# Kernel tuning notes

Hardware: AMD Instinct MI355X
Metric: run time of the kernel (lower is better)

Reference implementation:

```python
import jax, jax.numpy as jnp
import numpy as np

N_NODES = 50000
N_EDGES = 800000
NODE_DIM = 256
EDGE_DIM = 64
NUM_REL = 4
HID = 512      # hidden_dims[0]
LAST = 128     # last_dim_size
BATCH = 16384
EPS = 1e-10    # torchdrug RelationalGraphConv degree-normalization eps


def _glorot(k, shape):
    fan_in = shape[-1]
    return jax.random.normal(k, shape, jnp.float32) / np.sqrt(fan_in).astype(np.float32)


def setup_inputs() -> dict:
    key = jax.random.key(0)
    ks = jax.random.split(key, 20)
    inp = {}
    inp["inputs"] = jax.random.randint(ks[0], (BATCH, 3), 0, N_NODES, dtype=jnp.int32)
    inp["node_feature"] = jax.random.normal(ks[1], (N_NODES, NODE_DIM), jnp.float32)
    inp["edge_feature"] = jax.random.normal(ks[2], (N_EDGES, EDGE_DIM), jnp.float32)
    inp["edge_src"] = jax.random.randint(ks[3], (N_EDGES,), 0, N_NODES, dtype=jnp.int32)
    inp["edge_dst"] = jax.random.randint(ks[4], (N_EDGES,), 0, N_NODES, dtype=jnp.int32)
    inp["edge_rel"] = jax.random.randint(ks[5], (N_EDGES,), 0, NUM_REL, dtype=jnp.int32)
    # RGCN layer 1: 256 -> 512
    inp["We1"] = _glorot(ks[6], (NODE_DIM, EDGE_DIM)); inp["be1"] = jnp.zeros((NODE_DIM,), jnp.float32)
    inp["Wl1"] = _glorot(ks[7], (HID, NUM_REL * NODE_DIM)); inp["bl1"] = jnp.zeros((HID,), jnp.float32)
    inp["Ws1"] = _glorot(ks[8], (HID, NODE_DIM)); inp["bs1"] = jnp.zeros((HID,), jnp.float32)
    # RGCN layer 2: 512 -> 128
    inp["We2"] = _glorot(ks[9], (HID, EDGE_DIM)); inp["be2"] = jnp.zeros((HID,), jnp.float32)
    inp["Wl2"] = _glorot(ks[10], (LAST, NUM_REL * HID)); inp["bl2"] = jnp.zeros((LAST,), jnp.float32)
    inp["Ws2"] = _glorot(ks[11], (LAST, HID)); inp["bs2"] = jnp.zeros((LAST,), jnp.float32)
    # ccle_mlp: edge_dim -> 256 -> 128
    inp["Wc1"] = _glorot(ks[12], (256, EDGE_DIM)); inp["bc1"] = jnp.zeros((256,), jnp.float32)
    inp["Wc2"] = _glorot(ks[13], (LAST, 256)); inp["bc2"] = jnp.zeros((LAST,), jnp.float32)
    # final MLP: 3*128 -> 128 -> 64 -> 1
    inp["Wf1"] = _glorot(ks[14], (128, 3 * LAST)); inp["bf1"] = jnp.zeros((128,), jnp.float32)
    inp["Wf2"] = _glorot(ks[15], (64, 128)); inp["bf2"] = jnp.zeros((64,), jnp.float32)
    inp["Wf3"] = _glorot(ks[16], (1, 64)); inp["bf3"] = jnp.zeros((1,), jnp.float32)
    return inp


def _rgcn_layer(x, edge_src, edge_dst, edge_rel, edge_feat, We, be, Wl, bl, Ws, bs):
    """torchdrug RelationalGraphConv: message = x[src] + edge_linear(edge_feat);
    per-(node,relation) mean aggregation; combine = linear(update) + self_loop(x); relu."""
    in_dim = x.shape[1]
    msg = x[edge_src] + edge_feat @ We.T + be                      # [E, in_dim]
    seg = edge_dst * NUM_REL + edge_rel                            # [E]
    agg = jax.ops.segment_sum(msg, seg, num_segments=N_NODES * NUM_REL)
    cnt = jax.ops.segment_sum(jnp.ones((msg.shape[0], 1), msg.dtype), seg,
                              num_segments=N_NODES * NUM_REL)
    upd = (agg / (cnt + EPS)).reshape(N_NODES, NUM_REL * in_dim)   # [N, R*in_dim]
    return jax.nn.relu(upd @ Wl.T + bl + x @ Ws.T + bs)


def reference(inputs, node_feature, edge_feature, edge_src, edge_dst, edge_rel,
              We1, be1, Wl1, bl1, Ws1, bs1,
              We2, be2, Wl2, bl2, Ws2, bs2,
              Wc1, bc1, Wc2, bc2,
              Wf1, bf1, Wf2, bf2, Wf3, bf3):
    d1, d2, ctx = inputs[:, 0], inputs[:, 1], inputs[:, 2]
    h = _rgcn_layer(node_feature, edge_src, edge_dst, edge_rel, edge_feature,
                    We1, be1, Wl1, bl1, Ws1, bs1)
    h = _rgcn_layer(h, edge_src, edge_dst, edge_rel, edge_feature,
                    We2, be2, Wl2, bl2, Ws2, bs2)
    x1 = h[d1]                                                     # [B, 128]
    x2 = h[d2]                                                     # [B, 128]
    ef = edge_feature[ctx]                                         # [B, 64]
    x3 = jax.nn.relu(ef @ Wc1.T + bc1) @ Wc2.T + bc2               # [B, 128]
    x = jnp.concatenate([x1, x2, x3], axis=1)                      # [B, 384]
    x = jax.nn.relu(x @ Wf1.T + bf1)
    x = jax.nn.relu(x @ Wf2.T + bf2)
    return x @ Wf3.T + bf3                                         # [B, 1]
```

## Files before the change

kernel.cpp:

```cpp
#include <hip/hip_runtime.h>
#include <hip/hip_bf16.h>

#define N_NODES 50000
#define N_EDGES 800000
#define NODE_DIM 256
#define EDGE_DIM 64
#define NUM_REL 4
#define HID 512
#define LAST 128
#define BATCH 16384
#define EPS 1e-10f
#define NSEG (N_NODES * NUM_REL)

#define K1 1600
#define K2 832

typedef __bf16 bf16_t;
typedef __attribute__((ext_vector_type(8))) __bf16 bf16x8;
typedef __attribute__((ext_vector_type(4))) __bf16 bf16x4;
typedef __attribute__((ext_vector_type(2))) __bf16 bf16x2;
typedef __attribute__((ext_vector_type(4))) float f32x4;

typedef __attribute__((address_space(1))) const unsigned int g_u32;
typedef __attribute__((address_space(3))) unsigned int l_u32;
static __device__ __forceinline__ void gload16(const void* g, void* l) {
    __builtin_amdgcn_global_load_lds((g_u32*)g, (l_u32*)l, 16, 0, 0);
}

__global__ __launch_bounds__(256) void hist_kernel(
    const int* __restrict__ edst, const int* __restrict__ erel, int* __restrict__ hist)
{
    int e = blockIdx.x * 256 + threadIdx.x;
    if (e >= N_EDGES) return;
    atomicAdd(&hist[edst[e] * NUM_REL + erel[e]], 1);
}

#define SCAN_B 2048
__global__ __launch_bounds__(256) void scan1(
    const int* __restrict__ in, int* __restrict__ out, int* __restrict__ bsum, int n)
{
    __shared__ int sh[256];
    int base = blockIdx.x * SCAN_B + threadIdx.x * 8;
    int v[8]; int s = 0;
#pragma unroll
    for (int i = 0; i < 8; ++i) {
        int idx = base + i;
        v[i] = s;
        s += (idx < n) ? in[idx] : 0;
    }
    sh[threadIdx.x] = s;
    __syncthreads();
    for (int off = 1; off < 256; off <<= 1) {
        int t = (threadIdx.x >= off) ? sh[threadIdx.x - off] : 0;
        __syncthreads();
        sh[threadIdx.x] += t;
        __syncthreads();
    }
    int texcl = (threadIdx.x == 0) ? 0 : sh[threadIdx.x - 1];
#pragma unroll
    for (int i = 0; i < 8; ++i) {
        int idx = base + i;
        if (idx < n) out[idx] = texcl + v[i];
    }
    if (threadIdx.x == 255) bsum[blockIdx.x] = sh[255];
}

__global__ void scan2(int* bsum, int nb)
{
    if (threadIdx.x == 0 && blockIdx.x == 0) {
        int s = 0;
        for (int i = 0; i < nb; ++i) { int t = bsum[i]; bsum[i] = s; s += t; }
    }
}

__global__ __launch_bounds__(256) void scan3(int* __restrict__ out, const int* __restrict__ bsum, int n)
{
    int idx = blockIdx.x * SCAN_B + threadIdx.x * 8;
    int add = bsum[blockIdx.x];
#pragma unroll
    for (int i = 0; i < 8; ++i)
        if (idx + i < n) out[idx + i] += add;
}

__global__ __launch_bounds__(256) void csr_fill(
    const int* __restrict__ edst, const int* __restrict__ erel, const int* __restrict__ esrc,
    const int* __restrict__ offs, int* __restrict__ cursor,
    int* __restrict__ csr_src, int* __restrict__ csr_eid)
{
    int e = blockIdx.x * 256 + threadIdx.x;
    if (e >= N_EDGES) return;
    int seg = edst[e] * NUM_REL + erel[e];
    int pos = offs[seg] + atomicAdd(&cursor[seg], 1);
    csr_src[pos] = esrc[e];
    csr_eid[pos] = e;
}

__global__ __launch_bounds__(256) void prep_small(
    const float* __restrict__ Wc1, const float* __restrict__ Wc2,
    const float* __restrict__ Wf1, const float* __restrict__ Wf2,
    const float* __restrict__ bl1, const float* __restrict__ bs1,
    const float* __restrict__ bl2, const float* __restrict__ bs2,
    bf16_t* __restrict__ Wc1b, bf16_t* __restrict__ Wc2b,
    bf16_t* __restrict__ Wf1b, bf16_t* __restrict__ Wf2b,
    float* __restrict__ bias12, float* __restrict__ bias22)
{
    int i = blockIdx.x * 256 + threadIdx.x;
    const float* src; bf16_t* dst; int base;
    if (i < 4096)        { src = Wc1; dst = Wc1b; base = 0; }
    else if (i < 12288)  { src = Wc2; dst = Wc2b; base = 4096; }
    else if (i < 24576)  { src = Wf1; dst = Wf1b; base = 12288; }
    else if (i < 26624)  { src = Wf2; dst = Wf2b; base = 24576; }
    else {
        int j = i - 26624;
        if (j < 512) bias12[j] = bl1[j] + bs1[j];
        else if (j < 640) bias22[j - 512] = bl2[j - 512] + bs2[j - 512];
        return;
    }
    int k = i - base;
    float4 v = ((const float4*)src)[k];
    bf16x4 o;
    o[0] = (bf16_t)v.x; o[1] = (bf16_t)v.y; o[2] = (bf16_t)v.z; o[3] = (bf16_t)v.w;
    ((bf16x4*)dst)[k] = o;
}

__global__ __launch_bounds__(256) void xconv_k(const float* __restrict__ x, bf16_t* __restrict__ A1,
                                               bf16_t* __restrict__ xb)
{
    int i = blockIdx.x * 256 + threadIdx.x;
    int n = i >> 6;
    int c4 = i & 63;
    float4 v = ((const float4*)(x + (size_t)n * 256))[c4];
    bf16x4 o;
    o[0] = (bf16_t)v.x; o[1] = (bf16_t)v.y; o[2] = (bf16_t)v.z; o[3] = (bf16_t)v.w;
    *(bf16x4*)(A1 + (size_t)n * K1 + 1280 + c4 * 4) = o;
    *(bf16x4*)(xb + (size_t)n * 256 + c4 * 4) = o;
}

__global__ __launch_bounds__(256) void prep_w1cat(
    const float* __restrict__ Wl1, const float* __restrict__ We1,
    const float* __restrict__ Ws1, const float* __restrict__ be1, bf16_t* __restrict__ W1cat)
{
    int j = blockIdx.x;
    int t = threadIdx.x;
    const float* wrow = Wl1 + (size_t)j * 1024;
    bf16_t* out = W1cat + (size_t)j * K1;
    for (int c = t; c < 1024; c += 256) out[c] = (bf16_t)wrow[c];
    {
        int r = t >> 6, e = t & 63;
        float s = 0.f;
        const float* wr = wrow + r * 256;
        for (int c = 0; c < 256; ++c) s += wr[c] * We1[c * 64 + e];
        out[1024 + t] = (bf16_t)s;
    }
    if (t < 256) out[1280 + t] = (bf16_t)Ws1[(size_t)j * 256 + t];
    if (t < 4) {
        float s = 0.f;
        const float* wr = wrow + t * 256;
        for (int c = 0; c < 256; ++c) s += wr[c] * be1[c];
        out[1536 + t] = (bf16_t)s;
    }
    if (t >= 4 && t < 64) out[1536 + t] = (bf16_t)0.f;
}

__global__ __launch_bounds__(256) void prep_w2cat(
    const float* __restrict__ Wl2, const float* __restrict__ We2,
    const float* __restrict__ Ws2, const float* __restrict__ be2, bf16_t* __restrict__ W2cat)
{
    int j = blockIdx.x;
    int t = threadIdx.x;
    const float* wrow = Wl2 + (size_t)j * 2048;
    bf16_t* out = W2cat + (size_t)j * K2;
    {
        int r = t >> 6, e = t & 63;
        float s = 0.f;
        const float* wr = wrow + r * 512;
        for (int k = 0; k < 512; ++k) s += wr[k] * We2[k * 64 + e];
        out[t] = (bf16_t)s;
    }
    for (int c = t; c < 512; c += 256) out[256 + c] = (bf16_t)Ws2[(size_t)j * 512 + c];
    if (t < 4) {
        float s = 0.f;
        const float* wr = wrow + t * 512;
        for (int k = 0; k < 512; ++k) s += wr[k] * be2[k];
        out[768 + t] = (bf16_t)s;
    }
    if (t >= 4 && t < 64) out[768 + t] = (bf16_t)0.f;
}

__global__ __launch_bounds__(256) void prep_w2p(const float* __restrict__ Wl2, bf16_t* __restrict__ W2p)
{
    int idx = blockIdx.x * 256 + threadIdx.x;
    int row = idx >> 9, k = idx & 511;
    int j = row & 127, r = row >> 7;
    W2p[idx] = (bf16_t)Wl2[(size_t)j * 2048 + r * 512 + k];
}

__global__ __launch_bounds__(256) void agg1(
    const float* __restrict__ ef, const bf16_t* __restrict__ xb,
    const int* __restrict__ csr_src, const int* __restrict__ csr_eid,
    const int* __restrict__ offs, const int* __restrict__ hist,
    bf16_t* __restrict__ A1, bf16_t* __restrict__ A2)
{
    int n = blockIdx.x;
    int w = threadIdx.x >> 6;
    int lane = threadIdx.x & 63;
    int half = lane >> 5;
    int l32 = lane & 31;
    int seg = n * NUM_REL + w;
    int beg = offs[seg], ct = hist[seg];

    float xs[8] = {0.f, 0.f, 0.f, 0.f, 0.f, 0.f, 0.f, 0.f};
    float es0 = 0.f, es1 = 0.f;

    int i = 0;
    for (; i + 4 <= ct; i += 4) {
        int sA = csr_src[beg + i + half];
        int sB = csr_src[beg + i + 2 + half];
        int eA = csr_eid[beg + i + half];
        int eB = csr_eid[beg + i + 2 + half];
        bf16x8 vA = *(const bf16x8*)(xb + (size_t)sA * 256 + l32 * 8);
        bf16x8 vB = *(const bf16x8*)(xb + (size_t)sB * 256 + l32 * 8);
        float2 fA = *(const float2*)(ef + (size_t)eA * 64 + l32 * 2);
        float2 fB = *(const float2*)(ef + (size_t)eB * 64 + l32 * 2);
#pragma unroll
        for (int j = 0; j < 8; ++j) xs[j] += (float)vA[j] + (float)vB[j];
        es0 += fA.x + fB.x;
        es1 += fA.y + fB.y;
    }
    for (; i + 2 <= ct; i += 2) {
        int sA = csr_src[beg + i + half];
        int eA = csr_eid[beg + i + half];
        bf16x8 vA = *(const bf16x8*)(xb + (size_t)sA * 256 + l32 * 8);
        float2 fA = *(const float2*)(ef + (size_t)eA * 64 + l32 * 2);
#pragma unroll
        for (int j = 0; j < 8; ++j) xs[j] += (float)vA[j];
        es0 += fA.x;
        es1 += fA.y;
    }
    if (i < ct && half == 0) {
        int sA = csr_src[beg + i];
        int eA = csr_eid[beg + i];
        bf16x8 vA = *(const bf16x8*)(xb + (size_t)sA * 256 + l32 * 8);
        float2 fA = *(const float2*)(ef + (size_t)eA * 64 + l32 * 2);
#pragma unroll
        for (int j = 0; j < 8; ++j) xs[j] += (float)vA[j];
        es0 += fA.x;
        es1 += fA.y;
    }
#pragma unroll
    for (int j = 0; j < 8; ++j) xs[j] += __shfl_xor(xs[j], 32);
    es0 += __shfl_xor(es0, 32);
    es1 += __shfl_xor(es1, 32);

    float inv = 1.0f / ((float)ct + EPS);
    if (half == 0) {
        bf16x8 m;
#pragma unroll
        for (int j = 0; j < 8; ++j) m[j] = (bf16_t)(xs[j] * inv);
        *(bf16x8*)(A1 + (size_t)n * K1 + w * 256 + l32 * 8) = m;
        bf16x2 e2;
        e2[0] = (bf16_t)(es0 * inv);
        e2[1] = (bf16_t)(es1 * inv);
        *(bf16x2*)(A1 + (size_t)n * K1 + 1024 + w * 64 + l32 * 2) = e2;
        *(bf16x2*)(A2 + (size_t)n * K2 + w * 64 + l32 * 2) = e2;
    }
    if (lane == 0) {
        bf16_t fv = (bf16_t)((float)ct * inv);
        A1[(size_t)n * K1 + 1536 + w] = fv;
        A2[(size_t)n * K2 + 768 + w] = fv;
    }
    if (w == 3 && lane >= 4) {
        A1[(size_t)n * K1 + 1536 + lane] = (bf16_t)0.f;
        A2[(size_t)n * K2 + 768 + lane] = (bf16_t)0.f;
    }
}

__global__ __launch_bounds__(256) void agg2(
    const bf16_t* __restrict__ P, const int* __restrict__ csr_src,
    const int* __restrict__ offs, const int* __restrict__ hist,
    float* __restrict__ h2base)
{
    __shared__ float red[4][128];
    int n = blockIdx.x;
    int w = threadIdx.x >> 6;
    int lane = threadIdx.x & 63;
    int half = lane >> 5;
    int l32 = lane & 31;
    int seg = n * NUM_REL + w;
    int beg = offs[seg], ct = hist[seg];

    float s0 = 0.f, s1 = 0.f, s2 = 0.f, s3 = 0.f;
    int i = 0;
    for (; i + 4 <= ct; i += 4) {
        int a = csr_src[beg + i + half];
        int b = csr_src[beg + i + 2 + half];
        bf16x4 va = *(const bf16x4*)(P + (size_t)a * HID + w * 128 + l32 * 4);
        bf16x4 vb = *(const bf16x4*)(P + (size_t)b * HID + w * 128 + l32 * 4);
        s0 += (float)va[0] + (float)vb[0];
        s1 += (float)va[1] + (float)vb[1];
        s2 += (float)va[2] + (float)vb[2];
        s3 += (float)va[3] + (float)vb[3];
    }
    for (; i + 2 <= ct; i += 2) {
        int a = csr_src[beg + i + half];
        bf16x4 va = *(const bf16x4*)(P + (size_t)a * HID + w * 128 + l32 * 4);
        s0 += (float)va[0]; s1 += (float)va[1]; s2 += (float)va[2]; s3 += (float)va[3];
    }
    if (i < ct && half == 0) {
        int a = csr_src[beg + i];
        bf16x4 va = *(const bf16x4*)(P + (size_t)a * HID + w * 128 + l32 * 4);
        s0 += (float)va[0]; s1 += (float)va[1]; s2 += (float)va[2]; s3 += (float)va[3];
    }
    s0 += __shfl_xor(s0, 32);
    s1 += __shfl_xor(s1, 32);
    s2 += __shfl_xor(s2, 32);
    s3 += __shfl_xor(s3, 32);

    float inv = 1.0f / ((float)ct + EPS);
    if (half == 0) {
        red[w][l32 * 4 + 0] = s0 * inv;
        red[w][l32 * 4 + 1] = s1 * inv;
        red[w][l32 * 4 + 2] = s2 * inv;
        red[w][l32 * 4 + 3] = s3 * inv;
    }
    __syncthreads();
    int t = threadIdx.x;
    if (t < 128)
        h2base[(size_t)n * 128 + t] = red[0][t] + red[1][t] + red[2][t] + red[3][t];
}

template<int RELU, int ACC, int OUTBF>
__global__ __launch_bounds__(256) void gemm_bf16(
    const bf16_t* __restrict__ A, int lda,
    const bf16_t* __restrict__ W, int ldw,
    const float* __restrict__ Cin, int ldcin,
    const float* __restrict__ bias,
    void* __restrict__ Cout, int ldc,
    int M, int N, int K, int ncol)
{
    __shared__ char smem[32768];
    char* As = smem;
    char* Bs = smem + 16384;
    const int tid = threadIdx.x;

    const int nwg = gridDim.x;
    const int q8 = nwg >> 3, r8 = nwg & 7;
    const int xcd = blockIdx.x & 7, li = blockIdx.x >> 3;
    const int wgid = (xcd < r8 ? xcd * (q8 + 1) : r8 * (q8 + 1) + (xcd - r8) * q8) + li;

    const int row0 = (wgid / ncol) * 128;
    const int col0 = (wgid % ncol) * 128;
    const int lane = tid & 63, wv = tid >> 6;

    const int rsub = lane >> 3;
    const int gchunk = (lane & 7) ^ rsub;
    const bf16_t* pa[4]; const bf16_t* pb[4];
    char* la[4]; char* lb[4];
#pragma unroll
    for (int s = 0; s < 4; ++s) {
        int q = wv * 4 + s;
        int ar = row0 + q * 8 + rsub; if (ar >= M) ar = M - 1;
        int br = col0 + q * 8 + rsub; if (br >= N) br = N - 1;
        pa[s] = A + (size_t)ar * lda + gchunk * 8;
        pb[s] = W + (size_t)br * ldw + gchunk * 8;
        la[s] = As + q * 1024;
        lb[s] = Bs + q * 1024;
    }

    const int wm = wv >> 1, wn = wv & 1;
    const int r16 = lane & 15, kch = lane >> 4;
    const int sw = r16 & 7;

    f32x4 acc[4][4];
#pragma unroll
    for (int i = 0; i < 4; ++i)
#pragma unroll
        for (int j = 0; j < 4; ++j) acc[i][j] = (f32x4){0.f, 0.f, 0.f, 0.f};

    for (int k0 = 0; k0 < K; k0 += 64) {
#pragma unroll
        for (int s = 0; s < 4; ++s) {
            gload16(pa[s] + k0, la[s]);
            gload16(pb[s] + k0, lb[s]);
        }
        __syncthreads();
#pragma unroll
        for (int t = 0; t < 2; ++t) {
            const int slot = ((t * 4 + kch) ^ sw) << 4;
            bf16x8 af[4], bfm[4];
#pragma unroll
            for (int i = 0; i < 4; ++i)
                af[i] = *(const bf16x8*)(As + (wm * 64 + i * 16 + r16) * 128 + slot);
#pragma unroll
            for (int j = 0; j < 4; ++j)
                bfm[j] = *(const bf16x8*)(Bs + (wn * 64 + j * 16 + r16) * 128 + slot);
#pragma unroll
            for (int i = 0; i < 4; ++i)
#pragma unroll
                for (int j = 0; j < 4; ++j)
                    acc[i][j] = __builtin_amdgcn_mfma_f32_16x16x32_bf16(af[i], bfm[j], acc[i][j], 0, 0, 0);
        }
        __syncthreads();
    }

    const int crow0 = row0 + wm * 64;
#pragma unroll
    for (int i = 0; i < 4; ++i) {
#pragma unroll
        for (int j = 0; j < 4; ++j) {
            int col = col0 + wn * 64 + j * 16 + r16;
            if (col >= N) continue;
            float bv = bias ? bias[col] : 0.f;
#pragma unroll
            for (int q = 0; q < 4; ++q) {
                int row = crow0 + i * 16 + kch * 4 + q;
                if (row >= M) continue;
                float v = acc[i][j][q] + bv;
                if (ACC) v += Cin[(size_t)row * ldcin + col];
                if (RELU) v = fmaxf(v, 0.f);
                if (OUTBF) ((bf16_t*)Cout)[(size_t)row * ldc + col] = (bf16_t)v;
                else       ((float*)Cout)[(size_t)row * ldc + col] = v;
            }
        }
    }
}

__global__ __launch_bounds__(256) void gather_head(
    const int* __restrict__ inputs, const bf16_t* __restrict__ h2,
    const float* __restrict__ ef, bf16_t* __restrict__ xcat, bf16_t* __restrict__ ef_g)
{
    int i = blockIdx.x;
    int t = threadIdx.x;
    int d1 = inputs[i * 3 + 0];
    int d2 = inputs[i * 3 + 1];
    int ctx = inputs[i * 3 + 2];
    if (t < 128) {
        xcat[(size_t)i * 384 + t] = h2[(size_t)d1 * LAST + t];
    } else {
        int c = t - 128;
        xcat[(size_t)i * 384 + 128 + c] = h2[(size_t)d2 * LAST + c];
    }
    if (t < 64) ef_g[(size_t)i * 64 + t] = (bf16_t)ef[(size_t)ctx * EDGE_DIM + t];
}

__global__ __launch_bounds__(256) void final_matvec(
    const bf16_t* __restrict__ f2, const float* __restrict__ Wf3,
    const float* __restrict__ bf3, float* __restrict__ out, int M)
{
    int row = blockIdx.x * 4 + (threadIdx.x >> 6);
    int lane = threadIdx.x & 63;
    if (row >= M) return;
    float v = (float)f2[(size_t)row * 64 + lane] * Wf3[lane];
#pragma unroll
    for (int off = 32; off > 0; off >>= 1) v += __shfl_down(v, off);
    if (lane == 0) out[row] = v + bf3[0];
}

extern "C" void kernel_launch(void* const* d_in, const int* in_sizes, int n_in,
                              void* d_out, int out_size, void* d_ws, size_t ws_size,
                              hipStream_t stream)
{
    const int*   inputs       = (const int*)  d_in[0];
    const float* node_feature = (const float*)d_in[1];
    const float* edge_feature = (const float*)d_in[2];
    const int*   edge_src     = (const int*)  d_in[3];
    const int*   edge_dst     = (const int*)  d_in[4];
    const int*   edge_rel     = (const int*)  d_in[5];
    const float* We1 = (const float*)d_in[6];
    const float* be1 = (const float*)d_in[7];
    const float* Wl1 = (const float*)d_in[8];
    const float* bl1 = (const float*)d_in[9];
    const float* Ws1 = (const float*)d_in[10];
    const float* bs1 = (const float*)d_in[11];
    const float* We2 = (const float*)d_in[12];
    const float* be2 = (const float*)d_in[13];
    const float* Wl2 = (const float*)d_in[14];
    const float* bl2 = (const float*)d_in[15];
    const float* Ws2 = (const float*)d_in[16];
    const float* bs2 = (const float*)d_in[17];
    const float* Wc1 = (const float*)d_in[18];
    const float* bc1 = (const float*)d_in[19];
    const float* Wc2 = (const float*)d_in[20];
    const float* bc2 = (const float*)d_in[21];
    const float* Wf1 = (const float*)d_in[22];
    const float* bf1 = (const float*)d_in[23];
    const float* Wf2 = (const float*)d_in[24];
    const float* bf2 = (const float*)d_in[25];
    const float* Wf3 = (const float*)d_in[26];
    const float* bf3 = (const float*)d_in[27];
    float* out = (float*)d_out;

    char* p = (char*)d_ws;
    auto alloc = [&](size_t bytes) { char* r = p; p += (bytes + 255) & ~(size_t)255; return r; };
    int* hist     = (int*)alloc(NSEG * 4);
    int* offs     = (int*)alloc(NSEG * 4);
    int* cursor   = (int*)alloc(NSEG * 4);
    int* csr_src  = (int*)alloc(N_EDGES * 4);
    int* csr_eid  = (int*)alloc(N_EDGES * 4);
    int* bsums    = (int*)alloc(128 * 4);
    bf16_t* A1    = (bf16_t*)alloc((size_t)N_NODES * K1 * 2);
    bf16_t* A2    = (bf16_t*)alloc((size_t)N_NODES * K2 * 2);
    bf16_t* xb    = (bf16_t*)alloc((size_t)N_NODES * 256 * 2);
    bf16_t* Pbuf  = (bf16_t*)alloc((size_t)N_NODES * HID * 2);
    float*  h2base= (float*)alloc((size_t)N_NODES * 128 * 4);
    bf16_t* h2    = (bf16_t*)alloc((size_t)N_NODES * 128 * 2);
    bf16_t* W1cat = (bf16_t*)alloc((size_t)512 * K1 * 2);
    bf16_t* W2cat = (bf16_t*)alloc((size_t)128 * K2 * 2);
    bf16_t* W2p   = (bf16_t*)alloc((size_t)512 * 512 * 2);
    bf16_t* Wc1b  = (bf16_t*)alloc(256 * 64 * 2);
    bf16_t* Wc2b  = (bf16_t*)alloc(128 * 256 * 2);
    bf16_t* Wf1b  = (bf16_t*)alloc(128 * 384 * 2);
    bf16_t* Wf2b  = (bf16_t*)alloc(64 * 128 * 2);
    float*  bias12= (float*)alloc(512 * 4);
    float*  bias22= (float*)alloc(128 * 4);
    bf16_t* ef_g  = (bf16_t*)alloc((size_t)BATCH * 64 * 2);
    bf16_t* u3    = (bf16_t*)alloc((size_t)BATCH * 256 * 2);
    bf16_t* xcat  = (bf16_t*)alloc((size_t)BATCH * 384 * 2);
    bf16_t* f1    = (bf16_t*)alloc((size_t)BATCH * 128 * 2);
    bf16_t* f2    = (bf16_t*)alloc((size_t)BATCH * 64 * 2);

    hipMemsetAsync(hist, 0, NSEG * 4, stream);
    hipMemsetAsync(cursor, 0, NSEG * 4, stream);
    hist_kernel<<<(N_EDGES + 255) / 256, 256, 0, stream>>>(edge_dst, edge_rel, hist);
    int nscan = (NSEG + SCAN_B - 1) / SCAN_B;
    scan1<<<nscan, 256, 0, stream>>>(hist, offs, bsums, NSEG);
    scan2<<<1, 64, 0, stream>>>(bsums, nscan);
    scan3<<<nscan, 256, 0, stream>>>(offs, bsums, NSEG);
    csr_fill<<<(N_EDGES + 255) / 256, 256, 0, stream>>>(edge_dst, edge_rel, edge_src,
                                                        offs, cursor, csr_src, csr_eid);

    prep_w1cat<<<512, 256, 0, stream>>>(Wl1, We1, Ws1, be1, W1cat);
    prep_w2cat<<<128, 256, 0, stream>>>(Wl2, We2, Ws2, be2, W2cat);
    prep_w2p<<<(512 * 512) / 256, 256, 0, stream>>>(Wl2, W2p);
    prep_small<<<(26624 + 640 + 255) / 256, 256, 0, stream>>>(
        Wc1, Wc2, Wf1, Wf2, bl1, bs1, bl2, bs2,
        Wc1b, Wc2b, Wf1b, Wf2b, bias12, bias22);
    xconv_k<<<(N_NODES * 64 + 255) / 256, 256, 0, stream>>>(node_feature, A1, xb);

    agg1<<<N_NODES, 256, 0, stream>>>(edge_feature, xb, csr_src, csr_eid, offs, hist, A1, A2);
    {
        int nrow = (N_NODES + 127) / 128, ncol = HID / 128;
        gemm_bf16<1, 0, 1><<<nrow * ncol, 256, 0, stream>>>(A1, K1, W1cat, K1, nullptr, 0, bias12,
                                                            A2 + 256, K2, N_NODES, HID, K1, ncol);
    }

    {
        int nrow = (N_NODES + 127) / 128, ncol = HID / 128;
        gemm_bf16<0, 0, 1><<<nrow * ncol, 256, 0, stream>>>(A2 + 256, K2, W2p, 512, nullptr, 0, nullptr,
                                                            Pbuf, HID, N_NODES, HID, 512, ncol);
    }
    agg2<<<N_NODES, 256, 0, stream>>>(Pbuf, csr_src, offs, hist, h2base);
    {
        int nrow = (N_NODES + 127) / 128;
        gemm_bf16<1, 1, 1><<<nrow, 256, 0, stream>>>(A2, K2, W2cat, K2, h2base, 128, bias22,
                                                     h2, 128, N_NODES, 128, K2, 1);
    }

    gather_head<<<BATCH, 256, 0, stream>>>(inputs, h2, edge_feature, xcat, ef_g);
    {
        gemm_bf16<1, 0, 1><<<(BATCH / 128) * 2, 256, 0, stream>>>(ef_g, 64, Wc1b, 64, nullptr, 0, bc1,
                                                                  u3, 256, BATCH, 256, 64, 2);
    }
    {
        gemm_bf16<0, 0, 1><<<BATCH / 128, 256, 0, stream>>>(u3, 256, Wc2b, 256, nullptr, 0, bc2,
                                                            xcat + 256, 384, BATCH, 128, 256, 1);
    }
    {
        gemm_bf16<1, 0, 1><<<BATCH / 128, 256, 0, stream>>>(xcat, 384, Wf1b, 384, nullptr, 0, bf1,
                                                            f1, 128, BATCH, 128, 384, 1);
    }
    {
        gemm_bf16<1, 0, 1><<<BATCH / 128, 256, 0, stream>>>(f1, 128, Wf2b, 128, nullptr, 0, bf2,
                                                            f2, 64, BATCH, 64, 128, 1);
    }
    final_matvec<<<BATCH / 4, 256, 0, stream>>>(f2, Wf3, bf3, out, BATCH);
}
```

Baseline: 728.0 us.

## Double-buffer LDS tiles in bf16 GEMM to overlap global loads with MFMA

The GEMM kernel now holds two 32 KB LDS buffers and prefetches the next K-tile with direct global-to-LDS loads while the current tile is consumed by MFMA. Explicit vmcnt waits and raw s_barrier calls replace __syncthreads, so load latency can overlap compute. The cost is doubled LDS use, 64 KB per block, which lowers occupancy. Correctness relies on the hand-written waitcnt counts.

```diff
diff --git a/kernel.cpp b/kernel.cpp
--- a/kernel.cpp
+++ b/kernel.cpp
@@ -338,9 +338,7 @@
     void* __restrict__ Cout, int ldc,
     int M, int N, int K, int ncol)
 {
-    __shared__ char smem[32768];
-    char* As = smem;
-    char* Bs = smem + 16384;
+    __shared__ char smem[65536];
     const int tid = threadIdx.x;
 
     const int nwg = gridDim.x;
@@ -355,7 +353,7 @@
     const int rsub = lane >> 3;
     const int gchunk = (lane & 7) ^ rsub;
     const bf16_t* pa[4]; const bf16_t* pb[4];
-    char* la[4]; char* lb[4];
+    int lofs[4];
 #pragma unroll
     for (int s = 0; s < 4; ++s) {
         int q = wv * 4 + s;
@@ -363,8 +361,7 @@
         int br = col0 + q * 8 + rsub; if (br >= N) br = N - 1;
         pa[s] = A + (size_t)ar * lda + gchunk * 8;
         pb[s] = W + (size_t)br * ldw + gchunk * 8;
-        la[s] = As + q * 1024;
-        lb[s] = Bs + q * 1024;
+        lofs[s] = q * 1024;
     }
 
     const int wm = wv >> 1, wn = wv & 1;
@@ -377,13 +374,31 @@
 #pragma unroll
         for (int j = 0; j < 4; ++j) acc[i][j] = (f32x4){0.f, 0.f, 0.f, 0.f};
 
-    for (int k0 = 0; k0 < K; k0 += 64) {
-#pragma unroll
-        for (int s = 0; s < 4; ++s) {
-            gload16(pa[s] + k0, la[s]);
-            gload16(pb[s] + k0, lb[s]);
+#pragma unroll
+    for (int s = 0; s < 4; ++s) {
+        gload16(pa[s], smem + lofs[s]);
+        gload16(pb[s], smem + 16384 + lofs[s]);
+    }
+
+    const int nk = K >> 6;
+    int cur = 0;
+    for (int it = 0; it < nk; ++it) {
+        const int k0 = it << 6;
+        if (it + 1 < nk) {
+            char* nb = smem + ((cur ^ 1) << 15);
+#pragma unroll
+            for (int s = 0; s < 4; ++s) {
+                gload16(pa[s] + k0 + 64, nb + lofs[s]);
+                gload16(pb[s] + k0 + 64, nb + 16384 + lofs[s]);
+            }
+            asm volatile("s_waitcnt vmcnt(8)" ::: "memory");
+        } else {
+            asm volatile("s_waitcnt vmcnt(0)" ::: "memory");
         }
-        __syncthreads();
+        __builtin_amdgcn_s_barrier();
+        __builtin_amdgcn_sched_barrier(0);
+        const char* As = smem + (cur << 15);
+        const char* Bs = As + 16384;
 #pragma unroll
         for (int t = 0; t < 2; ++t) {
             const int slot = ((t * 4 + kch) ^ sw) << 4;
@@ -400,7 +415,8 @@
                 for (int j = 0; j < 4; ++j)
                     acc[i][j] = __builtin_amdgcn_mfma_f32_16x16x32_bf16(af[i], bfm[j], acc[i][j], 0, 0, 0);
         }
-        __syncthreads();
+        __builtin_amdgcn_s_barrier();
+        cur ^= 1;
     }
 
     const int crow0 = row0 + wm * 64;
```

Measured after the change: 705.5 us. -3.1%, faster.
